# Kernel optimization log

Hardware: AMD Instinct MI355X
Metric: run time of the kernel (lower is better)

The kernel has to match this reference:

```python
import jax, jax.numpy as jnp
import numpy as np

B, S, D_MODEL, D_K, D_V = 8, 2048, 1024, 1024, 1024


def setup_inputs() -> dict:
    key = jax.random.key(0)
    k1, k2, k3, k4 = jax.random.split(key, 4)
    x = jax.random.normal(k1, (B, S, D_MODEL), dtype=jnp.float32)
    # Store projection weights as [d_model, d_out] so projection is x @ W
    # (equivalent to torch Linear(d_model, d_out, bias=False) with W^T).
    scale = 1.0 / np.sqrt(D_MODEL)
    Wq = jax.random.normal(k2, (D_MODEL, D_K), dtype=jnp.float32) * scale
    Wk = jax.random.normal(k3, (D_MODEL, D_K), dtype=jnp.float32) * scale
    Wv = jax.random.normal(k4, (D_MODEL, D_V), dtype=jnp.float32) * scale
    return {"x": x, "Wq": Wq, "Wk": Wk, "Wv": Wv}


def reference(x, Wq, Wk, Wv):
    # Single-head causal self-attention, faithful to the original:
    # NOTE: the original scales by sqrt(x.shape[-1]) == sqrt(d_model),
    # not sqrt(d_k of the projection).
    Q = jnp.einsum('bsd,dk->bsk', x, Wq)
    K = jnp.einsum('bsd,dk->bsk', x, Wk)
    V = jnp.einsum('bsd,dv->bsv', x, Wv)
    inv_scale = 1.0 / jnp.sqrt(jnp.asarray(x.shape[-1], x.dtype))
    A = jnp.einsum('bqk,bsk->bqs', Q, K) * inv_scale  # [B, S, S]
    S_len = A.shape[-1]
    causal = jnp.tril(jnp.ones((S_len, S_len), dtype=bool))  # [S, S]
    A = jnp.where(causal, A, -jnp.inf)
    P = jax.nn.softmax(A, axis=-1)
    return jnp.einsum('bqs,bsv->bqv', P, V)
```

## Files before the change

### kernel.cpp

```cpp
#include <hip/hip_runtime.h>
#include <hip/hip_bf16.h>
#include <stdint.h>


typedef __bf16 bf16_t;
typedef __bf16 bf16x4 __attribute__((ext_vector_type(4)));
typedef __bf16 bf16x8 __attribute__((ext_vector_type(8)));
typedef float  floatx4 __attribute__((ext_vector_type(4)));

#define NB 8
#define SS 2048
#define DD 1024
#define INV_SCALE 0.03125f

__device__ __forceinline__ void async_ld16(const void* g, void* l) {
  __builtin_amdgcn_global_load_lds(
      (const __attribute__((address_space(1))) void*)g,
      (__attribute__((address_space(3))) void*)l, 16, 0, 0);
}

__device__ __forceinline__ void mm256_core(
    const bf16_t* __restrict__ Ab, const bf16_t* __restrict__ Bb,
    int lda, int ldb, int nt,
    bf16_t* sA0, bf16_t* sA1, bf16_t* sA2, bf16_t* sA3,
    bf16_t* sB0, bf16_t* sB1, bf16_t* sB2, bf16_t* sB3,
    floatx4 acc[8][4]) {
  const int t    = threadIdx.x;
  const int lane = t & 63;
  const int wid  = t >> 6;
  const int wm   = wid >> 2;
  const int wn   = wid & 3;
  const int fm   = lane & 15;
  const int q    = lane >> 4;
  const int co   = (q ^ ((fm >> 1) & 3)) * 8;

  size_t goA[2], goB[2]; int lo[2];
#pragma unroll
  for (int k = 0; k < 2; ++k) {
    const int u   = k * 512 + t;
    const int row = u >> 2;
    const int cg  = (u & 3) ^ ((row >> 1) & 3);
    goA[k] = (size_t)row * lda + cg * 8;
    goB[k] = (size_t)row * ldb + cg * 8;
    lo[k]  = u * 8;
  }

  auto stage = [&](bf16_t* la, bf16_t* lb, int tile) {
    const size_t ko = (size_t)tile * 32;
    async_ld16(Ab + ko + goA[0], la + lo[0]);
    async_ld16(Ab + ko + goA[1], la + lo[1]);
    async_ld16(Bb + ko + goB[0], lb + lo[0]);
    async_ld16(Bb + ko + goB[1], lb + lo[1]);
  };

  const int paOff = (wm * 128 + fm) * 32;
  const int pbOff = (wn * 64 + fm) * 32;

  auto body = [&] __attribute__((always_inline)) (
      const bf16_t* AP, const bf16_t* BP, bf16_t* AN, bf16_t* BN, int T) {
    if (T + 3 < nt) {
      stage(AN, BN, T + 3);
      asm volatile("s_waitcnt vmcnt(12)" ::: "memory");
    } else if (T + 2 < nt) {
      asm volatile("s_waitcnt vmcnt(8)" ::: "memory");
    } else if (T + 1 < nt) {
      asm volatile("s_waitcnt vmcnt(4)" ::: "memory");
    } else {
      asm volatile("s_waitcnt vmcnt(0)" ::: "memory");
    }
    __builtin_amdgcn_s_barrier();
    asm volatile("" ::: "memory");

    const bf16_t* pa = AP + paOff;
    const bf16_t* pb = BP + pbOff;
    bf16x8 a0[4], a1[4], bv[4];
#pragma unroll
    for (int i = 0; i < 4; ++i) a0[i] = *(const bf16x8*)(pa + i * 512 + co);
#pragma unroll
    for (int j = 0; j < 4; ++j) bv[j] = *(const bf16x8*)(pb + j * 512 + co);
    __builtin_amdgcn_sched_barrier(0);
#pragma unroll
    for (int i = 0; i < 4; ++i) a1[i] = *(const bf16x8*)(pa + (4 + i) * 512 + co);

    asm volatile("s_waitcnt lgkmcnt(4)" ::: "memory");
    __builtin_amdgcn_sched_barrier(0);
    __builtin_amdgcn_s_setprio(1);
#pragma unroll
    for (int i = 0; i < 4; ++i)
#pragma unroll
      for (int j = 0; j < 4; ++j)
        acc[i][j] = __builtin_amdgcn_mfma_f32_16x16x32_bf16(bv[j], a0[i], acc[i][j], 0, 0, 0);
    __builtin_amdgcn_s_setprio(0);

    asm volatile("s_waitcnt lgkmcnt(0)" ::: "memory");
    __builtin_amdgcn_sched_barrier(0);
    __builtin_amdgcn_s_setprio(1);
#pragma unroll
    for (int i = 0; i < 4; ++i)
#pragma unroll
      for (int j = 0; j < 4; ++j)
        acc[4 + i][j] = __builtin_amdgcn_mfma_f32_16x16x32_bf16(bv[j], a1[i], acc[4 + i][j], 0, 0, 0);
    __builtin_amdgcn_s_setprio(0);
    asm volatile("" ::: "memory");
    __builtin_amdgcn_s_barrier();
  };

  stage(sA0, sB0, 0);
  stage(sA1, sB1, 1);
  stage(sA2, sB2, 2);

  for (int tb = 0; tb < nt; tb += 4) {
    body(sA0, sB0, sA3, sB3, tb + 0);
    body(sA1, sB1, sA0, sB0, tb + 1);
    body(sA2, sB2, sA1, sB1, tb + 2);
    body(sA3, sB3, sA2, sB2, tb + 3);
  }
}

__device__ __forceinline__ void zero_acc8(floatx4 acc[8][4]) {
#pragma unroll
  for (int i = 0; i < 8; ++i)
#pragma unroll
    for (int j = 0; j < 4; ++j)
      acc[i][j] = floatx4{0.f, 0.f, 0.f, 0.f};
}

__device__ __forceinline__ void store_c256_bf16(bf16_t* __restrict__ Cb, int ldc,
                                                floatx4 acc[8][4]) {
  const int lane = threadIdx.x & 63;
  const int wid  = threadIdx.x >> 6;
  const int wm = wid >> 2, wn = wid & 3;
  const int m0 = wm * 128 + (lane & 15);
  const int n0 = wn * 64 + (lane >> 4) * 4;
#pragma unroll
  for (int i = 0; i < 8; ++i)
#pragma unroll
    for (int j = 0; j < 4; ++j) {
      floatx4 a = acc[i][j];
      bf16x4 o = {(bf16_t)a[0], (bf16_t)a[1], (bf16_t)a[2], (bf16_t)a[3]};
      *(bf16x4*)(Cb + (size_t)(m0 + i * 16) * ldc + n0 + j * 16) = o;
    }
}

#define MM256_LDS_DECL                                                      \
  __shared__ __attribute__((aligned(16))) bf16_t sA0[8192], sA1[8192],      \
      sA2[8192], sA3[8192];                                                 \
  __shared__ __attribute__((aligned(16))) bf16_t sB0[8192], sB1[8192],      \
      sB2[8192], sB3[8192];

__device__ __forceinline__ void mm_core(const bf16_t* __restrict__ Ab,
                                        const bf16_t* __restrict__ Bb,
                                        int lda, int ldb, int kTiles,
                                        bf16_t* sA, bf16_t* sB,
                                        floatx4 acc[4][4]) {
  const int t    = threadIdx.x;
  const int lane = t & 63;
  const int wm   = (t >> 6) >> 1;
  const int wn   = (t >> 6) & 1;
  const int fm   = lane & 15;
  const int q    = lane >> 4;
  const int xo   = fm & 7;

  const bf16_t* ga[4]; const bf16_t* gb[4];
  bf16_t* la[4]; bf16_t* lb[4];
#pragma unroll
  for (int k = 0; k < 4; ++k) {
    const int u   = k * 256 + t;
    const int row = u >> 3;
    const int cc  = (u & 7) ^ (row & 7);
    ga[k] = Ab + (size_t)row * lda + cc * 8;
    gb[k] = Bb + (size_t)row * ldb + cc * 8;
    la[k] = sA + u * 8;
    lb[k] = sB + u * 8;
  }

  const bf16_t* pa = sA + (wm * 64 + fm) * 64;
  const bf16_t* pb = sB + (wn * 64 + fm) * 64;

  for (int kt = 0; kt < kTiles; ++kt) {
    const int ko = kt * 64;
#pragma unroll
    for (int k = 0; k < 4; ++k) async_ld16(ga[k] + ko, la[k]);
#pragma unroll
    for (int k = 0; k < 4; ++k) async_ld16(gb[k] + ko, lb[k]);
    __syncthreads();
#pragma unroll
    for (int h = 0; h < 2; ++h) {
      const int co = ((h * 4 + q) ^ xo) * 8;
      bf16x8 af[4], bfr[4];
#pragma unroll
      for (int i = 0; i < 4; ++i) af[i]  = *(const bf16x8*)(pa + i * 1024 + co);
#pragma unroll
      for (int j = 0; j < 4; ++j) bfr[j] = *(const bf16x8*)(pb + j * 1024 + co);
#pragma unroll
      for (int i = 0; i < 4; ++i)
#pragma unroll
        for (int j = 0; j < 4; ++j)
          acc[i][j] = __builtin_amdgcn_mfma_f32_16x16x32_bf16(bfr[j], af[i], acc[i][j], 0, 0, 0);
    }
    __syncthreads();
  }
}

__device__ __forceinline__ void zero_acc(floatx4 acc[4][4]) {
#pragma unroll
  for (int i = 0; i < 4; ++i)
#pragma unroll
    for (int j = 0; j < 4; ++j)
      acc[i][j] = floatx4{0.f, 0.f, 0.f, 0.f};
}


__global__ __launch_bounds__(256) void prep(const float* __restrict__ x,
                                            const float* __restrict__ Wq,
                                            const float* __restrict__ Wk,
                                            const float* __restrict__ Wv,
                                            bf16_t* __restrict__ xb,
                                            bf16_t* __restrict__ Wt) {
  __shared__ float tile[32][33];
  const int bid = blockIdx.x;
  const int t = threadIdx.x;
  if (bid < 16384) {
    size_t i = (size_t)bid * 256 + t;
    float4 v = ((const float4*)x)[i];
    bf16x4 o = {(bf16_t)v.x, (bf16_t)v.y, (bf16_t)v.z, (bf16_t)v.w};
    ((bf16x4*)xb)[i] = o;
  } else {
    const int wb = bid - 16384;
    const int z = wb >> 10;
    const int rem = wb & 1023;
    const float* W = (z == 0) ? Wq : (z == 1 ? Wk : Wv);
    bf16_t* O = Wt + (size_t)z * DD * DD;
    const int ty = t >> 3;
    const int tx = t & 7;
    const int k0 = (rem >> 5) * 32, n0 = (rem & 31) * 32;
    float4 v = *(const float4*)(W + (size_t)(k0 + ty) * DD + n0 + tx * 4);
    tile[ty][tx * 4 + 0] = v.x;
    tile[ty][tx * 4 + 1] = v.y;
    tile[ty][tx * 4 + 2] = v.z;
    tile[ty][tx * 4 + 3] = v.w;
    __syncthreads();
    bf16x4 o = {(bf16_t)tile[tx * 4 + 0][ty], (bf16_t)tile[tx * 4 + 1][ty],
                (bf16_t)tile[tx * 4 + 2][ty], (bf16_t)tile[tx * 4 + 3][ty]};
    *(bf16x4*)(O + (size_t)(n0 + ty) * DD + k0 + tx * 4) = o;
  }
}


__global__ __launch_bounds__(512, 2) void qkproj_gemm(
    const bf16_t* __restrict__ xb, const bf16_t* __restrict__ Wt,
    bf16_t* __restrict__ QKb) {
  MM256_LDS_DECL
  const int mt = blockIdx.x, nt = blockIdx.y;
  const bf16_t* Ab = xb + (size_t)mt * 256 * DD;
  const bf16_t* Bb = Wt + (size_t)nt * 256 * DD;
  bf16_t* Cb = QKb + (size_t)mt * 256 * (2 * DD) + nt * 256;
  floatx4 acc[8][4];
  zero_acc8(acc);
  mm256_core(Ab, Bb, DD, DD, DD / 32,
             sA0, sA1, sA2, sA3, sB0, sB1, sB2, sB3, acc);
  store_c256_bf16(Cb, 2 * DD, acc);
}


__global__ __launch_bounds__(512, 2) void vproj_gemm(
    const bf16_t* __restrict__ xb, const bf16_t* __restrict__ Wt,
    bf16_t* __restrict__ VtB) {
  MM256_LDS_DECL
  const int bid = blockIdx.x;
  const int n = bid & 7;
  const int m = (bid >> 3) & 3;
  const int b = bid >> 5;
  const bf16_t* Ab = Wt + (size_t)2 * DD * DD + (size_t)m * 256 * DD;
  const bf16_t* Bb = xb + (size_t)b * SS * DD + (size_t)n * 256 * DD;
  bf16_t* Cb = VtB + (size_t)b * DD * SS + (size_t)m * 256 * SS + n * 256;
  floatx4 acc[8][4];
  zero_acc8(acc);
  mm256_core(Ab, Bb, DD, DD, DD / 32,
             sA0, sA1, sA2, sA3, sB0, sB1, sB2, sB3, acc);
  store_c256_bf16(Cb, SS, acc);
}


__global__ __launch_bounds__(256) void qk_p(
    const bf16_t* __restrict__ Q, const bf16_t* __restrict__ K,
    bf16_t* __restrict__ P, float* __restrict__ lpart) {
  const int b  = blockIdx.x & 7;
  const int tt = 135 - (blockIdx.x >> 3);
  int qi = (int)((sqrtf(8.0f * tt + 1.0f) - 1.0f) * 0.5f);
  while ((qi + 1) * (qi + 2) / 2 <= tt) ++qi;
  while (qi * (qi + 1) / 2 > tt) --qi;
  const int ki = tt - qi * (qi + 1) / 2;

  __shared__ __attribute__((aligned(16))) bf16_t sA[128 * 64];
  __shared__ __attribute__((aligned(16))) bf16_t sB[128 * 64];
  __shared__ float reds[2][128];
  const bf16_t* Ab = Q + ((size_t)b * SS + qi * 128) * (size_t)(2 * DD);
  const bf16_t* Bb = K + ((size_t)b * SS + ki * 128) * (size_t)(2 * DD);
  floatx4 acc[4][4];
  zero_acc(acc);
  mm_core(Ab, Bb, 2 * DD, 2 * DD, DD / 64, sA, sB, acc);

  const int lane = threadIdx.x & 63;
  const int wm = (threadIdx.x >> 6) >> 1, wn = (threadIdx.x >> 6) & 1;
  const bool diag = (ki == qi);
  bf16_t* Pb = P + (size_t)b * SS * SS;
  const int qloc0 = wm * 64 + (lane & 15);
  const int kvb0  = wn * 64 + (lane >> 4) * 4;

#pragma unroll
  for (int i = 0; i < 4; ++i) {
    const int qrow = qloc0 + i * 16;
    float partial = 0.f;
#pragma unroll
    for (int j = 0; j < 4; ++j) {
      const int kvb = kvb0 + j * 16;
      floatx4 p;
#pragma unroll
      for (int r = 0; r < 4; ++r) {
        const float s = acc[i][j][r] * INV_SCALE;
        p[r] = (diag && (kvb + r) > qrow) ? 0.f : __expf(s);
        partial += p[r];
      }
      bf16x4 o = {(bf16_t)p[0], (bf16_t)p[1], (bf16_t)p[2], (bf16_t)p[3]};
      *(bf16x4*)(Pb + (size_t)(qi * 128 + qrow) * SS + ki * 128 + kvb) = o;
    }
    partial += __shfl_xor(partial, 16);
    partial += __shfl_xor(partial, 32);
    if ((lane >> 4) == 0) reds[wn][qrow] = partial;
  }
  __syncthreads();
  const int t = threadIdx.x;
  if (t < 128) {
    size_t row = (size_t)b * SS + qi * 128 + t;
    lpart[row * 16 + ki] = reds[0][t] + reds[1][t];
  }
}


__global__ __launch_bounds__(256) void pv_gemm(
    const bf16_t* __restrict__ P, const bf16_t* __restrict__ Vt,
    const float* __restrict__ lpart, float* __restrict__ Out) {
  const int bid = blockIdx.x;
  const int b  = bid & 7;
  const int nj = (bid >> 3) & 7;
  const int qi = 15 - (bid >> 6);

  __shared__ __attribute__((aligned(16))) bf16_t sA[128 * 64];
  __shared__ __attribute__((aligned(16))) bf16_t sB[128 * 64];
  __shared__ float sRl[128];
  const int t = threadIdx.x;
  if (t < 128) {
    const float* lp = lpart + ((size_t)b * SS + qi * 128 + t) * 16;
    float L = 0.f;
    for (int ci = 0; ci <= qi; ++ci) L += lp[ci];
    sRl[t] = 1.0f / L;
  }
  const bf16_t* Ab = P + (size_t)b * SS * SS + (size_t)qi * 128 * SS;
  const bf16_t* Bb = Vt + (size_t)b * DD * SS + (size_t)nj * 128 * SS;
  float* Cb = Out + (size_t)b * SS * DD + (size_t)qi * 128 * DD + nj * 128;
  floatx4 acc[4][4];
  zero_acc(acc);
  mm_core(Ab, Bb, SS, SS, (qi + 1) * 2, sA, sB, acc);
  const int lane = threadIdx.x & 63;
  const int wm = (threadIdx.x >> 6) >> 1, wn = (threadIdx.x >> 6) & 1;
  const int m0 = wm * 64 + (lane & 15);
  const int n0 = wn * 64 + (lane >> 4) * 4;
#pragma unroll
  for (int i2 = 0; i2 < 4; ++i2) {
    const float scale = sRl[m0 + i2 * 16];
    float* crow = Cb + (size_t)(m0 + i2 * 16) * DD + n0;
#pragma unroll
    for (int j = 0; j < 4; ++j) {
      floatx4 o = acc[i2][j];
      o[0] *= scale; o[1] *= scale; o[2] *= scale; o[3] *= scale;
      *(floatx4*)(crow + j * 16) = o;
    }
  }
}


extern "C" void kernel_launch(void* const* d_in, const int* in_sizes, int n_in,
                              void* d_out, int out_size, void* d_ws, size_t ws_size,
                              hipStream_t stream) {
  const float* x  = (const float*)d_in[0];
  const float* Wq = (const float*)d_in[1];
  const float* Wk = (const float*)d_in[2];
  const float* Wv = (const float*)d_in[3];
  float* out = (float*)d_out;

  char* ws = (char*)d_ws;
  bf16_t* xb   = (bf16_t*)(ws);
  bf16_t* Wt   = (bf16_t*)(ws + 33554432ull);
  bf16_t* QKb  = (bf16_t*)(ws + 39845888ull);
  bf16_t* VtB  = (bf16_t*)(ws + 106954752ull);
  bf16_t* Pb   = (bf16_t*)(ws + 140509184ull);
  float*  lpart= (float*)(ws + 207618048ull);
  (void)in_sizes; (void)n_in; (void)out_size; (void)ws_size;

  prep<<<16384 + 3072, 256, 0, stream>>>(x, Wq, Wk, Wv, xb, Wt);
  qkproj_gemm<<<dim3(64, 8), 512, 0, stream>>>(xb, Wt, QKb);
  vproj_gemm<<<256, 512, 0, stream>>>(xb, Wt, VtB);
  qk_p<<<1088, 256, 0, stream>>>(QKb, QKb + DD, Pb, lpart);
  pv_gemm<<<1024, 256, 0, stream>>>(Pb, VtB, lpart, out);
}
```

Measured before the change: 353.3 us.

## Prefetch next tile's LDS fragments into registers during current MFMA block

Restructures the GEMM main loop to software-pipeline LDS-to-register loads. Each iteration issues the A/B fragments for the next K-tile into a ping-pong register set while MFMAs on the current tile run. One barrier per iteration replaces two. The global prefetch depth drops from three tiles ahead to two to make room for this. The aim is to hide LDS read latency behind the MFMAs. In exchange it uses more registers and has a shallower global-load pipeline, which may expose more memory latency.

```diff
diff --git a/kernel.cpp b/kernel.cpp
--- a/kernel.cpp
+++ b/kernel.cpp
@@ -18,6 +18,9 @@
       (const __attribute__((address_space(1))) void*)g,
       (__attribute__((address_space(3))) void*)l, 16, 0, 0);
 }
+
+#define BARRIER() do { asm volatile("" ::: "memory"); \
+  __builtin_amdgcn_s_barrier(); asm volatile("" ::: "memory"); } while (0)
 
 __device__ __forceinline__ void mm256_core(
     const bf16_t* __restrict__ Ab, const bf16_t* __restrict__ Bb,
@@ -56,64 +59,77 @@
   const int paOff = (wm * 128 + fm) * 32;
   const int pbOff = (wn * 64 + fm) * 32;
 
+  bf16x8 a0P[4], bvP[4], a0Q[4], bvQ[4], aT[4];
+
+  stage(sA0, sB0, 0);
+  stage(sA1, sB1, 1);
+  asm volatile("s_waitcnt vmcnt(4)" ::: "memory");
+  BARRIER();
+  {
+    const bf16_t* pa = sA0 + paOff;
+    const bf16_t* pb = sB0 + pbOff;
+#pragma unroll
+    for (int i = 0; i < 4; ++i) a0P[i] = *(const bf16x8*)(pa + i * 512 + co);
+#pragma unroll
+    for (int j = 0; j < 4; ++j) bvP[j] = *(const bf16x8*)(pb + j * 512 + co);
+  }
+
   auto body = [&] __attribute__((always_inline)) (
-      const bf16_t* AP, const bf16_t* BP, bf16_t* AN, bf16_t* BN, int T) {
-    if (T + 3 < nt) {
-      stage(AN, BN, T + 3);
-      asm volatile("s_waitcnt vmcnt(12)" ::: "memory");
-    } else if (T + 2 < nt) {
-      asm volatile("s_waitcnt vmcnt(8)" ::: "memory");
+      const bf16_t* CAp, const bf16_t* NAp, const bf16_t* NBp,
+      bf16_t* SAp, bf16_t* SBp,
+      bf16x8 (&ca0)[4], bf16x8 (&cbv)[4],
+      bf16x8 (&na0)[4], bf16x8 (&nbv)[4], int T) {
+    if (T + 2 < nt) {
+      stage(SAp, SBp, T + 2);
+      asm volatile("s_waitcnt vmcnt(4)" ::: "memory");
     } else if (T + 1 < nt) {
-      asm volatile("s_waitcnt vmcnt(4)" ::: "memory");
+      asm volatile("s_waitcnt vmcnt(0)" ::: "memory");
+    }
+    BARRIER();
+
+    const bf16_t* pac = CAp + paOff;
+#pragma unroll
+    for (int i = 0; i < 4; ++i) aT[i] = *(const bf16x8*)(pac + (4 + i) * 512 + co);
+    if (T + 1 < nt) {
+      const bf16_t* pan = NAp + paOff;
+      const bf16_t* pbn = NBp + pbOff;
+#pragma unroll
+      for (int i = 0; i < 4; ++i) na0[i] = *(const bf16x8*)(pan + i * 512 + co);
+#pragma unroll
+      for (int j = 0; j < 4; ++j) nbv[j] = *(const bf16x8*)(pbn + j * 512 + co);
+      asm volatile("s_waitcnt lgkmcnt(12)" ::: "memory");
     } else {
-      asm volatile("s_waitcnt vmcnt(0)" ::: "memory");
-    }
-    __builtin_amdgcn_s_barrier();
-    asm volatile("" ::: "memory");
-
-    const bf16_t* pa = AP + paOff;
-    const bf16_t* pb = BP + pbOff;
-    bf16x8 a0[4], a1[4], bv[4];
-#pragma unroll
-    for (int i = 0; i < 4; ++i) a0[i] = *(const bf16x8*)(pa + i * 512 + co);
-#pragma unroll
-    for (int j = 0; j < 4; ++j) bv[j] = *(const bf16x8*)(pb + j * 512 + co);
-    __builtin_amdgcn_sched_barrier(0);
-#pragma unroll
-    for (int i = 0; i < 4; ++i) a1[i] = *(const bf16x8*)(pa + (4 + i) * 512 + co);
-
-    asm volatile("s_waitcnt lgkmcnt(4)" ::: "memory");
+      asm volatile("s_waitcnt lgkmcnt(4)" ::: "memory");
+    }
     __builtin_amdgcn_sched_barrier(0);
     __builtin_amdgcn_s_setprio(1);
 #pragma unroll
     for (int i = 0; i < 4; ++i)
 #pragma unroll
       for (int j = 0; j < 4; ++j)
-        acc[i][j] = __builtin_amdgcn_mfma_f32_16x16x32_bf16(bv[j], a0[i], acc[i][j], 0, 0, 0);
+        acc[i][j] = __builtin_amdgcn_mfma_f32_16x16x32_bf16(cbv[j], ca0[i], acc[i][j], 0, 0, 0);
     __builtin_amdgcn_s_setprio(0);
 
-    asm volatile("s_waitcnt lgkmcnt(0)" ::: "memory");
+    if (T + 1 < nt) {
+      asm volatile("s_waitcnt lgkmcnt(8)" ::: "memory");
+    } else {
+      asm volatile("s_waitcnt lgkmcnt(0)" ::: "memory");
+    }
     __builtin_amdgcn_sched_barrier(0);
     __builtin_amdgcn_s_setprio(1);
 #pragma unroll
     for (int i = 0; i < 4; ++i)
 #pragma unroll
       for (int j = 0; j < 4; ++j)
-        acc[4 + i][j] = __builtin_amdgcn_mfma_f32_16x16x32_bf16(bv[j], a1[i], acc[4 + i][j], 0, 0, 0);
+        acc[4 + i][j] = __builtin_amdgcn_mfma_f32_16x16x32_bf16(cbv[j], aT[i], acc[4 + i][j], 0, 0, 0);
     __builtin_amdgcn_s_setprio(0);
-    asm volatile("" ::: "memory");
-    __builtin_amdgcn_s_barrier();
   };
 
-  stage(sA0, sB0, 0);
-  stage(sA1, sB1, 1);
-  stage(sA2, sB2, 2);
-
-  for (int tb = 0; tb < nt; tb += 4) {
-    body(sA0, sB0, sA3, sB3, tb + 0);
-    body(sA1, sB1, sA0, sB0, tb + 1);
-    body(sA2, sB2, sA1, sB1, tb + 2);
-    body(sA3, sB3, sA2, sB2, tb + 3);
+  for (int T = 0; T < nt; T += 4) {
+    body(sA0,  sA1, sB1,  sA2, sB2,  a0P, bvP,  a0Q, bvQ, T + 0);
+    body(sA1,  sA2, sB2,  sA3, sB3,  a0Q, bvQ,  a0P, bvP, T + 1);
+    body(sA2,  sA3, sB3,  sA0, sB0,  a0P, bvP,  a0Q, bvQ, T + 2);
+    body(sA3,  sA0, sB0,  sA1, sB1,  a0Q, bvQ,  a0P, bvP, T + 3);
   }
 }
 
```

New measurement: 501.6 us. 42.0% more time.

## Double-buffer LDS tiles in 128x128 GEMM core with async prefetch

Applied to the files above, without the earlier changes.

Replaces the single-buffered mm_core, used by the QK^T/P and PV GEMMs, with mm_core2. The new core ping-pongs between two LDS buffers and issues the next tile's global-to-LDS loads before computing the current one, with explicit vmcnt waits and raw s_barrier. The aim is to hide global load latency behind the MFMA work instead of stalling on a load-then-sync each iteration. It also raises wave priority around the MFMA block. LDS use per block doubles, which may cut occupancy. The loop unrolls by two, so nt must be even; both call sites pass even tile counts.

```diff
diff --git a/kernel.cpp b/kernel.cpp
--- a/kernel.cpp
+++ b/kernel.cpp
@@ -18,6 +18,9 @@
       (const __attribute__((address_space(1))) void*)g,
       (__attribute__((address_space(3))) void*)l, 16, 0, 0);
 }
+
+#define BARRIER() do { asm volatile("" ::: "memory"); \
+  __builtin_amdgcn_s_barrier(); asm volatile("" ::: "memory"); } while (0)
 
 __device__ __forceinline__ void mm256_core(
     const bf16_t* __restrict__ Ab, const bf16_t* __restrict__ Bb,
@@ -148,11 +151,11 @@
   __shared__ __attribute__((aligned(16))) bf16_t sB0[8192], sB1[8192],      \
       sB2[8192], sB3[8192];
 
-__device__ __forceinline__ void mm_core(const bf16_t* __restrict__ Ab,
-                                        const bf16_t* __restrict__ Bb,
-                                        int lda, int ldb, int kTiles,
-                                        bf16_t* sA, bf16_t* sB,
-                                        floatx4 acc[4][4]) {
+__device__ __forceinline__ void mm_core2(
+    const bf16_t* __restrict__ Ab, const bf16_t* __restrict__ Bb,
+    int lda, int ldb, int nt,
+    bf16_t* sA0, bf16_t* sB0, bf16_t* sA1, bf16_t* sB1,
+    floatx4 acc[4][4]) {
   const int t    = threadIdx.x;
   const int lane = t & 63;
   const int wm   = (t >> 6) >> 1;
@@ -161,29 +164,40 @@
   const int q    = lane >> 4;
   const int xo   = fm & 7;
 
-  const bf16_t* ga[4]; const bf16_t* gb[4];
-  bf16_t* la[4]; bf16_t* lb[4];
+  size_t goA[4], goB[4]; int lo[4];
 #pragma unroll
   for (int k = 0; k < 4; ++k) {
     const int u   = k * 256 + t;
     const int row = u >> 3;
     const int cc  = (u & 7) ^ (row & 7);
-    ga[k] = Ab + (size_t)row * lda + cc * 8;
-    gb[k] = Bb + (size_t)row * ldb + cc * 8;
-    la[k] = sA + u * 8;
-    lb[k] = sB + u * 8;
-  }
-
-  const bf16_t* pa = sA + (wm * 64 + fm) * 64;
-  const bf16_t* pb = sB + (wn * 64 + fm) * 64;
-
-  for (int kt = 0; kt < kTiles; ++kt) {
-    const int ko = kt * 64;
-#pragma unroll
-    for (int k = 0; k < 4; ++k) async_ld16(ga[k] + ko, la[k]);
-#pragma unroll
-    for (int k = 0; k < 4; ++k) async_ld16(gb[k] + ko, lb[k]);
-    __syncthreads();
+    goA[k] = (size_t)row * lda + cc * 8;
+    goB[k] = (size_t)row * ldb + cc * 8;
+    lo[k]  = u * 8;
+  }
+
+  auto stage = [&](bf16_t* la, bf16_t* lb, int tile) {
+    const size_t ko = (size_t)tile * 64;
+#pragma unroll
+    for (int k = 0; k < 4; ++k) async_ld16(Ab + ko + goA[k], la + lo[k]);
+#pragma unroll
+    for (int k = 0; k < 4; ++k) async_ld16(Bb + ko + goB[k], lb + lo[k]);
+  };
+
+  const int paOff = (wm * 64 + fm) * 64;
+  const int pbOff = (wn * 64 + fm) * 64;
+
+  auto body = [&] __attribute__((always_inline)) (
+      const bf16_t* CA, const bf16_t* CB, bf16_t* SA, bf16_t* SB, int T) {
+    if (T + 1 < nt) {
+      stage(SA, SB, T + 1);
+      asm volatile("s_waitcnt vmcnt(8)" ::: "memory");
+    } else {
+      asm volatile("s_waitcnt vmcnt(0)" ::: "memory");
+    }
+    BARRIER();
+
+    const bf16_t* pa = CA + paOff;
+    const bf16_t* pb = CB + pbOff;
 #pragma unroll
     for (int h = 0; h < 2; ++h) {
       const int co = ((h * 4 + q) ^ xo) * 8;
@@ -192,13 +206,23 @@
       for (int i = 0; i < 4; ++i) af[i]  = *(const bf16x8*)(pa + i * 1024 + co);
 #pragma unroll
       for (int j = 0; j < 4; ++j) bfr[j] = *(const bf16x8*)(pb + j * 1024 + co);
+      asm volatile("s_waitcnt lgkmcnt(0)" ::: "memory");
+      __builtin_amdgcn_sched_barrier(0);
+      __builtin_amdgcn_s_setprio(1);
 #pragma unroll
       for (int i = 0; i < 4; ++i)
 #pragma unroll
         for (int j = 0; j < 4; ++j)
           acc[i][j] = __builtin_amdgcn_mfma_f32_16x16x32_bf16(bfr[j], af[i], acc[i][j], 0, 0, 0);
-    }
-    __syncthreads();
+      __builtin_amdgcn_s_setprio(0);
+    }
+    BARRIER();
+  };
+
+  stage(sA0, sB0, 0);
+  for (int T = 0; T < nt; T += 2) {
+    body(sA0, sB0, sA1, sB1, T);
+    body(sA1, sB1, sA0, sB0, T + 1);
   }
 }
 
@@ -209,6 +233,10 @@
     for (int j = 0; j < 4; ++j)
       acc[i][j] = floatx4{0.f, 0.f, 0.f, 0.f};
 }
+
+#define MM128_LDS_DECL                                                      \
+  __shared__ __attribute__((aligned(16))) bf16_t sA0[128 * 64], sA1[128 * 64]; \
+  __shared__ __attribute__((aligned(16))) bf16_t sB0[128 * 64], sB1[128 * 64];
 
 
 __global__ __launch_bounds__(256) void prep(const float* __restrict__ x,
@@ -292,14 +320,13 @@
   while (qi * (qi + 1) / 2 > tt) --qi;
   const int ki = tt - qi * (qi + 1) / 2;
 
-  __shared__ __attribute__((aligned(16))) bf16_t sA[128 * 64];
-  __shared__ __attribute__((aligned(16))) bf16_t sB[128 * 64];
+  MM128_LDS_DECL
   __shared__ float reds[2][128];
   const bf16_t* Ab = Q + ((size_t)b * SS + qi * 128) * (size_t)(2 * DD);
   const bf16_t* Bb = K + ((size_t)b * SS + ki * 128) * (size_t)(2 * DD);
   floatx4 acc[4][4];
   zero_acc(acc);
-  mm_core(Ab, Bb, 2 * DD, 2 * DD, DD / 64, sA, sB, acc);
+  mm_core2(Ab, Bb, 2 * DD, 2 * DD, DD / 64, sA0, sB0, sA1, sB1, acc);
 
   const int lane = threadIdx.x & 63;
   const int wm = (threadIdx.x >> 6) >> 1, wn = (threadIdx.x >> 6) & 1;
@@ -346,8 +373,7 @@
   const int nj = (bid >> 3) & 7;
   const int qi = 15 - (bid >> 6);
 
-  __shared__ __attribute__((aligned(16))) bf16_t sA[128 * 64];
-  __shared__ __attribute__((aligned(16))) bf16_t sB[128 * 64];
+  MM128_LDS_DECL
   __shared__ float sRl[128];
   const int t = threadIdx.x;
   if (t < 128) {
@@ -361,7 +387,7 @@
   float* Cb = Out + (size_t)b * SS * DD + (size_t)qi * 128 * DD + nj * 128;
   floatx4 acc[4][4];
   zero_acc(acc);
-  mm_core(Ab, Bb, SS, SS, (qi + 1) * 2, sA, sB, acc);
+  mm_core2(Ab, Bb, SS, SS, (qi + 1) * 2, sA0, sB0, sA1, sB1, acc);
   const int lane = threadIdx.x & 63;
   const int wm = (threadIdx.x >> 6) >> 1, wn = (threadIdx.x >> 6) & 1;
   const int m0 = wm * 64 + (lane & 15);
```

After: 351.1 us. No clear change (-0.6%).
